# Performance work log

Measured on AMD Instinct MI355X. Metric: run time of the kernel, lower is better.

## Reference

```python
import jax, jax.numpy as jnp
import numpy as np

B, T, C = 8, 2048, 1024
HEAD = 64


def setup_inputs() -> dict:
    key = jax.random.key(0)
    kx, kk, kq, kv = jax.random.split(key, 4)
    scale = 1.0 / np.sqrt(C)
    x = jax.random.normal(kx, (B, T, C), dtype=jnp.float32)
    # nn.Linear(n_embd, head_size, bias=False) weight shape: (head_size, n_embd)
    Wk = jax.random.normal(kk, (HEAD, C), dtype=jnp.float32) * scale
    Wq = jax.random.normal(kq, (HEAD, C), dtype=jnp.float32) * scale
    Wv = jax.random.normal(kv, (HEAD, C), dtype=jnp.float32) * scale
    return {"x": x, "Wk": Wk, "Wq": Wq, "Wv": Wv}


def reference(x, Wk, Wq, Wv):
    Bb, Tt, Cc = x.shape
    k = jnp.einsum('btc,hc->bth', x, Wk)  # (B,T,head)
    q = jnp.einsum('btc,hc->bth', x, Wq)
    v = jnp.einsum('btc,hc->bth', x, Wv)
    scaling = Cc ** (-0.5)  # NOTE: scales by full embed dim C, per source
    wei = jnp.einsum('bth,bsh->bts', q, k) * scaling  # (B,T,T)
    causal = jnp.tril(jnp.ones((Tt, Tt), dtype=bool))
    wei = jnp.where(causal, wei, -jnp.inf)
    wei = jax.nn.softmax(wei, axis=-1)  # stable max-subtract softmax (= _safe_softmax)
    out = jnp.einsum('bts,bsh->bth', wei, v)  # (B,T,head)
    return out
```

## Files before the change

### kernel.cpp

```cpp
#include <hip/hip_runtime.h>
#include <math.h>

#define B_ 8
#define T_ 2048
#define C_ 1024
#define H_ 64
#define M_ (B_ * T_)

typedef short bf8 __attribute__((ext_vector_type(8)));
typedef float f32x4 __attribute__((ext_vector_type(4)));

__device__ __forceinline__ unsigned short f2b(float f) {
    unsigned u = __float_as_uint(f);
    u += 0x7fffu + ((u >> 16) & 1u);
    return (unsigned short)(u >> 16);
}
__device__ __forceinline__ float b2f(unsigned short u) {
    return __uint_as_float(((unsigned)u) << 16);
}
__device__ __forceinline__ unsigned pack2(float lo, float hi) {
    unsigned a = __float_as_uint(lo) + 0x8000u;
    unsigned b = __float_as_uint(hi) + 0x8000u;
    return __builtin_amdgcn_perm(b, a, 0x07060302u);
}

__global__ __launch_bounds__(256) void wconv_kernel(
    const float* __restrict__ Wk, const float* __restrict__ Wq,
    const float* __restrict__ Wv, unsigned short* __restrict__ wP)
{
    int gid = blockIdx.x * 256 + threadIdx.x;
    int l   = gid & 63;
    int kk  = (gid >> 6) & 31;
    int jg  = gid >> 11;
    int m15 = l & 15, q4 = l >> 4;
    int n   = 16 * jg + m15;
    int c0  = 32 * kk + 8 * q4;
    const float* src;
    float scl;
    if (n < 64)       { src = Wq + (size_t)n * C_ + c0;        scl = 0.03125f; }
    else if (n < 128) { src = Wk + (size_t)(n - 64) * C_ + c0; scl = 1.0f; }
    else              { src = Wv + (size_t)(n - 128) * C_ + c0; scl = 1.0f; }
    float4 a = *(const float4*)src;
    float4 b = *(const float4*)(src + 4);
    ushort4 o0 = make_ushort4(f2b(a.x * scl), f2b(a.y * scl), f2b(a.z * scl), f2b(a.w * scl));
    ushort4 o1 = make_ushort4(f2b(b.x * scl), f2b(b.y * scl), f2b(b.z * scl), f2b(b.w * scl));
    *(ushort4*)(wP + (size_t)gid * 8)     = o0;
    *(ushort4*)(wP + (size_t)gid * 8 + 4) = o1;
}

__global__ __launch_bounds__(256) void qkv_kernel(
    const float* __restrict__ x, const unsigned short* __restrict__ wP,
    unsigned short* __restrict__ qo, unsigned short* __restrict__ kP,
    unsigned short* __restrict__ vP)
{
    __shared__ unsigned short As[2][32 * 64];

    const int tid  = threadIdx.x;
    const int lane = tid & 63;
    const int w    = tid >> 6;
    const int m15  = lane & 15;
    const int q4   = lane >> 4;
    const int r0   = blockIdx.x * 32;

    const int arow = tid >> 3;
    const int aoct = tid & 7;
    const float* xp = x + (size_t)(r0 + arow) * C_ + aoct * 8;
    const int awo = arow * 64 + ((aoct ^ (arow & 7)) * 8);

    const unsigned short* wbase = wP + ((size_t)(3 * w) * 2048 + lane) * 8;

    f32x4 acc[2][3];
#pragma unroll
    for (int i = 0; i < 2; ++i)
#pragma unroll
        for (int j = 0; j < 3; ++j) acc[i][j] = f32x4{0.f, 0.f, 0.f, 0.f};

    float4 xa0 = *(const float4*)xp;
    float4 xa1 = *(const float4*)(xp + 4);
    bf8 wreg[3][2];
#pragma unroll
    for (int j = 0; j < 3; ++j)
#pragma unroll
        for (int kc = 0; kc < 2; ++kc)
            wreg[j][kc] = *(const bf8*)(wbase + ((size_t)j * 2048 + kc * 64) * 8);

    {
        uint4 u = {pack2(xa0.x, xa0.y), pack2(xa0.z, xa0.w),
                   pack2(xa1.x, xa1.y), pack2(xa1.z, xa1.w)};
        *(uint4*)&As[0][awo] = u;
    }

    const int swz = m15 & 7;
    for (int ck = 0; ck < 16; ++ck) {
        const int nxt = ck + 1;
        float4 xb0, xb1;
        bf8 wn[3][2];
        if (nxt < 16) {
            xb0 = *(const float4*)(xp + nxt * 64);
            xb1 = *(const float4*)(xp + nxt * 64 + 4);
#pragma unroll
            for (int j = 0; j < 3; ++j)
#pragma unroll
                for (int kc = 0; kc < 2; ++kc)
                    wn[j][kc] = *(const bf8*)(wbase + ((size_t)j * 2048 + (2 * nxt + kc) * 64) * 8);
        }
        __syncthreads();
        const int buf = ck & 1;
#pragma unroll
        for (int kc = 0; kc < 2; ++kc) {
            bf8 af[2];
#pragma unroll
            for (int i = 0; i < 2; ++i)
                af[i] = *(const bf8*)&As[buf][(16 * i + m15) * 64 + (((4 * kc + q4) ^ swz) * 8)];
#pragma unroll
            for (int i = 0; i < 2; ++i)
#pragma unroll
                for (int j = 0; j < 3; ++j)
                    acc[i][j] = __builtin_amdgcn_mfma_f32_16x16x32_bf16(
                        af[i], wreg[j][kc], acc[i][j], 0, 0, 0);
        }
        if (nxt < 16) {
            uint4 u = {pack2(xb0.x, xb0.y), pack2(xb0.z, xb0.w),
                       pack2(xb1.x, xb1.y), pack2(xb1.z, xb1.w)};
            *(uint4*)&As[nxt & 1][awo] = u;
#pragma unroll
            for (int j = 0; j < 3; ++j)
#pragma unroll
                for (int kc = 0; kc < 2; ++kc) wreg[j][kc] = wn[j][kc];
        }
    }

#pragma unroll
    for (int i = 0; i < 2; ++i) {
#pragma unroll
        for (int j = 0; j < 3; ++j) {
            const int base = 48 * w + 16 * j;
            if (base < 64) {
#pragma unroll
                for (int r = 0; r < 4; ++r) {
                    int t = r0 + 16 * i + 4 * q4 + r;
                    qo[(size_t)t * H_ + base + m15] = f2b(acc[i][j][r]);
                }
            } else if (base < 128) {
                const int D0 = base - 64;
                const int f  = D0 >> 5;
                const int c1 = (D0 >> 3) & 3;
                const int l2 = (c1 + (m15 >> 3)) * 16;
#pragma unroll
                for (int r = 0; r < 4; ++r) {
                    int t  = r0 + 16 * i + 4 * q4 + r;
                    int bb = t >> 11, tt = t & 2047;
                    kP[(size_t)bb * 131072 +
                       (size_t)((((tt >> 4) * 2 + f) * 64 + l2 + (tt & 15)) * 8 + (m15 & 7))]
                        = f2b(acc[i][j][r]);
                }
            } else {
                const int cg = (base - 128) >> 4;
#pragma unroll
                for (int r = 0; r < 4; ++r) {
                    int t  = r0 + 16 * i + 4 * q4 + r;
                    int bb = t >> 11, tt = t & 2047;
                    int lv = ((tt & 31) >> 3) * 16 + m15;
                    vP[(size_t)bb * 131072 +
                       (size_t)((((tt >> 5) * 4 + cg) * 64 + lv) * 8 + (tt & 7))]
                        = f2b(acc[i][j][r]);
                }
            }
        }
    }
}

__global__ __launch_bounds__(512) void attn_kernel(
    const unsigned short* __restrict__ qo, const unsigned short* __restrict__ kP,
    const unsigned short* __restrict__ vP, float* __restrict__ outp)
{
    __shared__ unsigned short Pl[8][2][16 * 64];
    __shared__ float Ml[2][4][2][16];
    __shared__ unsigned short Ob[2][3][2][16 * 64];

    const int tid  = threadIdx.x;
    const int lane = tid & 63;
    const int w    = tid >> 6;
    const int m15  = lane & 15;
    const int q4   = lane >> 4;
    const int b    = blockIdx.x;
    const int y    = blockIdx.y;
    const int gsel = w >> 2;
    const int s    = w & 3;
    const int g    = gsel ? (63 - y) : y;
    const int trow = 32 * g;
    const int last = g >> 1;

    const unsigned short* qb = qo + (size_t)b * T_ * H_;
    const unsigned short* kb = kP + (size_t)b * 131072;
    const unsigned short* vb = vP + (size_t)b * 131072;

    bf8 qf[2][2];
#pragma unroll
    for (int gq = 0; gq < 2; ++gq)
#pragma unroll
        for (int f = 0; f < 2; ++f)
            qf[gq][f] = *(const bf8*)(qb + (size_t)(trow + 16 * gq + m15) * H_ + 32 * f + 8 * q4);

    f32x4 o[2][4];
#pragma unroll
    for (int gq = 0; gq < 2; ++gq)
#pragma unroll
        for (int cg = 0; cg < 4; ++cg) o[gq][cg] = f32x4{0.f, 0.f, 0.f, 0.f};
    float lr[2] = {0.f, 0.f};

    bf8 kf[4][2];
    if (s <= last) {
#pragma unroll
        for (int t2 = 0; t2 < 4; ++t2)
#pragma unroll
            for (int f = 0; f < 2; ++f)
                kf[t2][f] = *(const bf8*)(kb + (size_t)(((4 * s + t2) * 2 + f) * 64 + lane) * 8);
    }

    const int swz = m15 & 7;
    for (int kt = s; kt <= last; kt += 4) {
        const bool more = (kt + 4 <= last);
        bf8 kn[4][2];
        if (more) {
#pragma unroll
            for (int t2 = 0; t2 < 4; ++t2)
#pragma unroll
                for (int f = 0; f < 2; ++f)
                    kn[t2][f] = *(const bf8*)(kb + (size_t)(((4 * (kt + 4) + t2) * 2 + f) * 64 + lane) * 8);
        }
        bf8 vf[2][4];
#pragma unroll
        for (int kc = 0; kc < 2; ++kc)
#pragma unroll
            for (int cg = 0; cg < 4; ++cg)
                vf[kc][cg] = *(const bf8*)(vb + (size_t)(((2 * kt + kc) * 4 + cg) * 64 + lane) * 8);

#pragma unroll
        for (int gq = 0; gq < 2; ++gq) {
            f32x4 sa[4];
#pragma unroll
            for (int t2 = 0; t2 < 4; ++t2) sa[t2] = f32x4{0.f, 0.f, 0.f, 0.f};
#pragma unroll
            for (int t2 = 0; t2 < 4; ++t2)
#pragma unroll
                for (int f = 0; f < 2; ++f)
                    sa[t2] = __builtin_amdgcn_mfma_f32_16x16x32_bf16(
                        kf[t2][f], qf[gq][f], sa[t2], 0, 0, 0);

            if (kt == last) {
#pragma unroll
                for (int t2 = 0; t2 < 4; ++t2)
#pragma unroll
                    for (int r = 0; r < 4; ++r)
                        if (64 * kt + 16 * t2 + 4 * q4 + r > trow + 16 * gq + m15)
                            sa[t2][r] = -INFINITY;
            }

            float p[4][4];
            float sum = 0.f;
#pragma unroll
            for (int t2 = 0; t2 < 4; ++t2)
#pragma unroll
                for (int r = 0; r < 4; ++r) {
                    p[t2][r] = __expf(sa[t2][r]);
                    sum += p[t2][r];
                }
            lr[gq] += sum;

#pragma unroll
            for (int t2 = 0; t2 < 4; ++t2) {
                uint2 pk = {pack2(p[t2][0], p[t2][1]), pack2(p[t2][2], p[t2][3])};
                int c = 2 * t2 + (q4 >> 1);
                *(uint2*)&Pl[w][gq][m15 * 64 + ((c ^ swz) * 8) + (q4 & 1) * 4] = pk;
            }
            bf8 pf[2];
#pragma unroll
            for (int kc = 0; kc < 2; ++kc)
                pf[kc] = *(const bf8*)&Pl[w][gq][m15 * 64 + (((4 * kc + q4) ^ swz) * 8)];

#pragma unroll
            for (int cg = 0; cg < 4; ++cg) {
                o[gq][cg] = __builtin_amdgcn_mfma_f32_16x16x32_bf16(
                    pf[0], vf[0][cg], o[gq][cg], 0, 0, 0);
                o[gq][cg] = __builtin_amdgcn_mfma_f32_16x16x32_bf16(
                    pf[1], vf[1][cg], o[gq][cg], 0, 0, 0);
            }
        }

        if (more) {
#pragma unroll
            for (int t2 = 0; t2 < 4; ++t2)
#pragma unroll
                for (int f = 0; f < 2; ++f) kf[t2][f] = kn[t2][f];
        }
    }

#pragma unroll
    for (int gq = 0; gq < 2; ++gq) {
        lr[gq] += __shfl_xor(lr[gq], 16);
        lr[gq] += __shfl_xor(lr[gq], 32);
    }
    if (q4 == 0) {
#pragma unroll
        for (int gq = 0; gq < 2; ++gq) Ml[gsel][s][gq][m15] = lr[gq];
    }
    if (s >= 1) {
#pragma unroll
        for (int gq = 0; gq < 2; ++gq)
#pragma unroll
            for (int cg = 0; cg < 4; ++cg)
#pragma unroll
                for (int r = 0; r < 4; ++r)
                    Ob[gsel][s - 1][gq][(4 * q4 + r) * 64 + 16 * cg + m15] = f2b(o[gq][cg][r]);
    }
    __syncthreads();
    if (s == 0) {
        float* op = outp + (size_t)(b * T_ + trow) * H_;
#pragma unroll
        for (int gq = 0; gq < 2; ++gq) {
#pragma unroll
            for (int r = 0; r < 4; ++r) {
                const int qq = 4 * q4 + r;
                float L = Ml[gsel][0][gq][qq] + Ml[gsel][1][gq][qq]
                        + Ml[gsel][2][gq][qq] + Ml[gsel][3][gq][qq];
                float inv = 1.0f / L;
#pragma unroll
                for (int cg = 0; cg < 4; ++cg) {
                    float a = o[gq][cg][r];
#pragma unroll
                    for (int i = 1; i < 4; ++i)
                        a += b2f(Ob[gsel][i - 1][gq][qq * 64 + 16 * cg + m15]);
                    op[(size_t)(16 * gq + qq) * H_ + 16 * cg + m15] = a * inv;
                }
            }
        }
    }
}

extern "C" void kernel_launch(void* const* d_in, const int* in_sizes, int n_in,
                              void* d_out, int out_size, void* d_ws, size_t ws_size,
                              hipStream_t stream) {
    const float* x  = (const float*)d_in[0];
    const float* Wk = (const float*)d_in[1];
    const float* Wq = (const float*)d_in[2];
    const float* Wv = (const float*)d_in[3];
    char* ws = (char*)d_ws;
    unsigned short* wP = (unsigned short*)ws;
    unsigned short* qo = (unsigned short*)(ws + 0x080000);
    unsigned short* kP = (unsigned short*)(ws + 0x280000);
    unsigned short* vP = (unsigned short*)(ws + 0x480000);

    wconv_kernel<<<96, 256, 0, stream>>>(Wk, Wq, Wv, wP);
    qkv_kernel<<<M_ / 32, 256, 0, stream>>>(x, wP, qo, kP, vP);
    attn_kernel<<<dim3(8, 32), 512, 0, stream>>>(qo, kP, vP, (float*)d_out);
}
```

Measured before the change: 125.0 us.

## Fuse weight conversion, QKV projection and attention into one cooperative kernel

Merges the three kernels into a single cooperative kernel of 256 blocks with 512 threads, separated by grid-wide syncs, to remove two kernel launch gaps. The QKV stage is retiled so each block covers 64 rows with 8 waves instead of 32 rows with 4 waves, which adds an extra __syncthreads per k-step. Grid.sync costs and the reduced QKV parallelism (256 blocks instead of 512) may offset the launch savings.

```diff
diff --git a/kernel.cpp b/kernel.cpp
--- a/kernel.cpp
+++ b/kernel.cpp
@@ -1,5 +1,8 @@
 #include <hip/hip_runtime.h>
+#include <hip/hip_cooperative_groups.h>
 #include <math.h>
+
+namespace cg = cooperative_groups;
 
 #define B_ 8
 #define T_ 2048
@@ -24,314 +27,312 @@
     return __builtin_amdgcn_perm(b, a, 0x07060302u);
 }
 
-__global__ __launch_bounds__(256) void wconv_kernel(
-    const float* __restrict__ Wk, const float* __restrict__ Wq,
-    const float* __restrict__ Wv, unsigned short* __restrict__ wP)
+__global__ __launch_bounds__(512) void fused_kernel(
+    const float* __restrict__ x, const float* __restrict__ Wk,
+    const float* __restrict__ Wq, const float* __restrict__ Wv,
+    unsigned short* __restrict__ wP, unsigned short* __restrict__ qo,
+    unsigned short* __restrict__ kP, unsigned short* __restrict__ vP,
+    float* __restrict__ outp)
 {
-    int gid = blockIdx.x * 256 + threadIdx.x;
-    int l   = gid & 63;
-    int kk  = (gid >> 6) & 31;
-    int jg  = gid >> 11;
-    int m15 = l & 15, q4 = l >> 4;
-    int n   = 16 * jg + m15;
-    int c0  = 32 * kk + 8 * q4;
-    const float* src;
-    float scl;
-    if (n < 64)       { src = Wq + (size_t)n * C_ + c0;        scl = 0.03125f; }
-    else if (n < 128) { src = Wk + (size_t)(n - 64) * C_ + c0; scl = 1.0f; }
-    else              { src = Wv + (size_t)(n - 128) * C_ + c0; scl = 1.0f; }
-    float4 a = *(const float4*)src;
-    float4 b = *(const float4*)(src + 4);
-    ushort4 o0 = make_ushort4(f2b(a.x * scl), f2b(a.y * scl), f2b(a.z * scl), f2b(a.w * scl));
-    ushort4 o1 = make_ushort4(f2b(b.x * scl), f2b(b.y * scl), f2b(b.z * scl), f2b(b.w * scl));
-    *(ushort4*)(wP + (size_t)gid * 8)     = o0;
-    *(ushort4*)(wP + (size_t)gid * 8 + 4) = o1;
-}
-
-__global__ __launch_bounds__(256) void qkv_kernel(
-    const float* __restrict__ x, const unsigned short* __restrict__ wP,
-    unsigned short* __restrict__ qo, unsigned short* __restrict__ kP,
-    unsigned short* __restrict__ vP)
-{
-    __shared__ unsigned short As[2][32 * 64];
-
+    __shared__ unsigned short As[2][64 * 64];
+    __shared__ unsigned short Pl[8][2][16 * 64];
+    __shared__ float Ml[2][4][2][16];
+    __shared__ unsigned short Ob[2][3][2][16 * 64];
+
+    cg::grid_group grid = cg::this_grid();
+    const int bid  = blockIdx.x;
     const int tid  = threadIdx.x;
     const int lane = tid & 63;
     const int w    = tid >> 6;
     const int m15  = lane & 15;
     const int q4   = lane >> 4;
-    const int r0   = blockIdx.x * 32;
-
-    const int arow = tid >> 3;
-    const int aoct = tid & 7;
-    const float* xp = x + (size_t)(r0 + arow) * C_ + aoct * 8;
-    const int awo = arow * 64 + ((aoct ^ (arow & 7)) * 8);
-
-    const unsigned short* wbase = wP + ((size_t)(3 * w) * 2048 + lane) * 8;
-
-    f32x4 acc[2][3];
-#pragma unroll
-    for (int i = 0; i < 2; ++i)
-#pragma unroll
-        for (int j = 0; j < 3; ++j) acc[i][j] = f32x4{0.f, 0.f, 0.f, 0.f};
-
-    float4 xa0 = *(const float4*)xp;
-    float4 xa1 = *(const float4*)(xp + 4);
-    bf8 wreg[3][2];
-#pragma unroll
-    for (int j = 0; j < 3; ++j)
-#pragma unroll
-        for (int kc = 0; kc < 2; ++kc)
-            wreg[j][kc] = *(const bf8*)(wbase + ((size_t)j * 2048 + kc * 64) * 8);
 
     {
-        uint4 u = {pack2(xa0.x, xa0.y), pack2(xa0.z, xa0.w),
-                   pack2(xa1.x, xa1.y), pack2(xa1.z, xa1.w)};
-        *(uint4*)&As[0][awo] = u;
+        int gid = bid * 512 + tid;
+        if (gid < 24576) {
+            int l   = gid & 63;
+            int kk  = (gid >> 6) & 31;
+            int jg  = gid >> 11;
+            int n   = 16 * jg + (l & 15);
+            int c0  = 32 * kk + 8 * (l >> 4);
+            const float* src;
+            float scl;
+            if (n < 64)       { src = Wq + (size_t)n * C_ + c0;         scl = 0.03125f; }
+            else if (n < 128) { src = Wk + (size_t)(n - 64) * C_ + c0;  scl = 1.0f; }
+            else              { src = Wv + (size_t)(n - 128) * C_ + c0; scl = 1.0f; }
+            float4 a = *(const float4*)src;
+            float4 b = *(const float4*)(src + 4);
+            *(ushort4*)(wP + (size_t)gid * 8) =
+                make_ushort4(f2b(a.x * scl), f2b(a.y * scl), f2b(a.z * scl), f2b(a.w * scl));
+            *(ushort4*)(wP + (size_t)gid * 8 + 4) =
+                make_ushort4(f2b(b.x * scl), f2b(b.y * scl), f2b(b.z * scl), f2b(b.w * scl));
+        }
     }
-
-    const int swz = m15 & 7;
-    for (int ck = 0; ck < 16; ++ck) {
-        const int nxt = ck + 1;
-        float4 xb0, xb1;
-        bf8 wn[3][2];
-        if (nxt < 16) {
-            xb0 = *(const float4*)(xp + nxt * 64);
-            xb1 = *(const float4*)(xp + nxt * 64 + 4);
-#pragma unroll
-            for (int j = 0; j < 3; ++j)
+    grid.sync();
+
+    {
+        const int wr = w >> 2;
+        const int wc = w & 3;
+        const int r0 = bid * 64;
+
+        const int arow = tid >> 3;
+        const int aoct = tid & 7;
+        const float* xp = x + (size_t)(r0 + arow) * C_ + aoct * 8;
+        const int awo = arow * 64 + ((aoct ^ (arow & 7)) * 8);
+
+        const unsigned short* wbase = wP + ((size_t)(3 * wc) * 2048 + lane) * 8;
+
+        f32x4 acc[2][3];
+#pragma unroll
+        for (int i = 0; i < 2; ++i)
+#pragma unroll
+            for (int j = 0; j < 3; ++j) acc[i][j] = f32x4{0.f, 0.f, 0.f, 0.f};
+
+        float4 xa0 = *(const float4*)xp;
+        float4 xa1 = *(const float4*)(xp + 4);
+        bf8 wreg[3][2];
+#pragma unroll
+        for (int j = 0; j < 3; ++j)
+#pragma unroll
+            for (int kc = 0; kc < 2; ++kc)
+                wreg[j][kc] = *(const bf8*)(wbase + ((size_t)j * 2048 + kc * 64) * 8);
+
+        *(uint4*)&As[0][awo] = uint4{pack2(xa0.x, xa0.y), pack2(xa0.z, xa0.w),
+                                     pack2(xa1.x, xa1.y), pack2(xa1.z, xa1.w)};
+
+        const int swz = m15 & 7;
+        for (int ck = 0; ck < 16; ++ck) {
+            const int nxt = ck + 1;
+            float4 xb0, xb1;
+            bf8 wn[3][2];
+            if (nxt < 16) {
+                xb0 = *(const float4*)(xp + nxt * 64);
+                xb1 = *(const float4*)(xp + nxt * 64 + 4);
+#pragma unroll
+                for (int j = 0; j < 3; ++j)
+#pragma unroll
+                    for (int kc = 0; kc < 2; ++kc)
+                        wn[j][kc] = *(const bf8*)(wbase + ((size_t)j * 2048 + (2 * nxt + kc) * 64) * 8);
+            }
+            __syncthreads();
+            const int buf = ck & 1;
+#pragma unroll
+            for (int kc = 0; kc < 2; ++kc) {
+                bf8 af[2];
+#pragma unroll
+                for (int i = 0; i < 2; ++i)
+                    af[i] = *(const bf8*)&As[buf][(32 * wr + 16 * i + m15) * 64 +
+                                                  (((4 * kc + q4) ^ swz) * 8)];
+#pragma unroll
+                for (int i = 0; i < 2; ++i)
+#pragma unroll
+                    for (int j = 0; j < 3; ++j)
+                        acc[i][j] = __builtin_amdgcn_mfma_f32_16x16x32_bf16(
+                            af[i], wreg[j][kc], acc[i][j], 0, 0, 0);
+            }
+            if (nxt < 16) {
+                __syncthreads();
+                *(uint4*)&As[nxt & 1][awo] = uint4{pack2(xb0.x, xb0.y), pack2(xb0.z, xb0.w),
+                                                   pack2(xb1.x, xb1.y), pack2(xb1.z, xb1.w)};
+#pragma unroll
+                for (int j = 0; j < 3; ++j)
+#pragma unroll
+                    for (int kc = 0; kc < 2; ++kc) wreg[j][kc] = wn[j][kc];
+            }
+        }
+
+#pragma unroll
+        for (int i = 0; i < 2; ++i) {
+#pragma unroll
+            for (int j = 0; j < 3; ++j) {
+                const int base = 48 * wc + 16 * j;
+                if (base < 64) {
+#pragma unroll
+                    for (int r = 0; r < 4; ++r) {
+                        int t = r0 + 32 * wr + 16 * i + 4 * q4 + r;
+                        qo[(size_t)t * H_ + base + m15] = f2b(acc[i][j][r]);
+                    }
+                } else if (base < 128) {
+                    const int D0 = base - 64;
+                    const int f  = D0 >> 5;
+                    const int c1 = (D0 >> 3) & 3;
+                    const int l2 = (c1 + (m15 >> 3)) * 16;
+#pragma unroll
+                    for (int r = 0; r < 4; ++r) {
+                        int t  = r0 + 32 * wr + 16 * i + 4 * q4 + r;
+                        int bb = t >> 11, tt = t & 2047;
+                        kP[(size_t)bb * 131072 +
+                           (size_t)((((tt >> 4) * 2 + f) * 64 + l2 + (tt & 15)) * 8 + (m15 & 7))]
+                            = f2b(acc[i][j][r]);
+                    }
+                } else {
+                    const int cg2 = (base - 128) >> 4;
+#pragma unroll
+                    for (int r = 0; r < 4; ++r) {
+                        int t  = r0 + 32 * wr + 16 * i + 4 * q4 + r;
+                        int bb = t >> 11, tt = t & 2047;
+                        int lv = ((tt & 31) >> 3) * 16 + m15;
+                        vP[(size_t)bb * 131072 +
+                           (size_t)((((tt >> 5) * 4 + cg2) * 64 + lv) * 8 + (tt & 7))]
+                            = f2b(acc[i][j][r]);
+                    }
+                }
+            }
+        }
+    }
+    grid.sync();
+
+    {
+        const int b    = bid & 7;
+        const int y    = bid >> 3;
+        const int gsel = w >> 2;
+        const int s    = w & 3;
+        const int g    = gsel ? (63 - y) : y;
+        const int trow = 32 * g;
+        const int last = g >> 1;
+
+        const unsigned short* qb = qo + (size_t)b * T_ * H_;
+        const unsigned short* kb = kP + (size_t)b * 131072;
+        const unsigned short* vb = vP + (size_t)b * 131072;
+
+        bf8 qf[2][2];
+#pragma unroll
+        for (int gq = 0; gq < 2; ++gq)
+#pragma unroll
+            for (int f = 0; f < 2; ++f)
+                qf[gq][f] = *(const bf8*)(qb + (size_t)(trow + 16 * gq + m15) * H_ + 32 * f + 8 * q4);
+
+        f32x4 o[2][4];
+#pragma unroll
+        for (int gq = 0; gq < 2; ++gq)
+#pragma unroll
+            for (int cg2 = 0; cg2 < 4; ++cg2) o[gq][cg2] = f32x4{0.f, 0.f, 0.f, 0.f};
+        float lr[2] = {0.f, 0.f};
+
+        bf8 kf[4][2];
+        if (s <= last) {
+#pragma unroll
+            for (int t2 = 0; t2 < 4; ++t2)
+#pragma unroll
+                for (int f = 0; f < 2; ++f)
+                    kf[t2][f] = *(const bf8*)(kb + (size_t)(((4 * s + t2) * 2 + f) * 64 + lane) * 8);
+        }
+
+        const int swz = m15 & 7;
+        for (int kt = s; kt <= last; kt += 4) {
+            const bool more = (kt + 4 <= last);
+            bf8 kn[4][2];
+            if (more) {
+#pragma unroll
+                for (int t2 = 0; t2 < 4; ++t2)
+#pragma unroll
+                    for (int f = 0; f < 2; ++f)
+                        kn[t2][f] = *(const bf8*)(kb + (size_t)(((4 * (kt + 4) + t2) * 2 + f) * 64 + lane) * 8);
+            }
+            bf8 vf[2][4];
+#pragma unroll
+            for (int kc = 0; kc < 2; ++kc)
+#pragma unroll
+                for (int cg2 = 0; cg2 < 4; ++cg2)
+                    vf[kc][cg2] = *(const bf8*)(vb + (size_t)(((2 * kt + kc) * 4 + cg2) * 64 + lane) * 8);
+
+#pragma unroll
+            for (int gq = 0; gq < 2; ++gq) {
+                f32x4 sa[4];
+#pragma unroll
+                for (int t2 = 0; t2 < 4; ++t2) sa[t2] = f32x4{0.f, 0.f, 0.f, 0.f};
+#pragma unroll
+                for (int t2 = 0; t2 < 4; ++t2)
+#pragma unroll
+                    for (int f = 0; f < 2; ++f)
+                        sa[t2] = __builtin_amdgcn_mfma_f32_16x16x32_bf16(
+                            kf[t2][f], qf[gq][f], sa[t2], 0, 0, 0);
+
+                if (kt == last) {
+#pragma unroll
+                    for (int t2 = 0; t2 < 4; ++t2)
+#pragma unroll
+                        for (int r = 0; r < 4; ++r)
+                            if (64 * kt + 16 * t2 + 4 * q4 + r > trow + 16 * gq + m15)
+                                sa[t2][r] = -INFINITY;
+                }
+
+                float p[4][4];
+                float sum = 0.f;
+#pragma unroll
+                for (int t2 = 0; t2 < 4; ++t2)
+#pragma unroll
+                    for (int r = 0; r < 4; ++r) {
+                        p[t2][r] = __expf(sa[t2][r]);
+                        sum += p[t2][r];
+                    }
+                lr[gq] += sum;
+
+#pragma unroll
+                for (int t2 = 0; t2 < 4; ++t2) {
+                    uint2 pk = {pack2(p[t2][0], p[t2][1]), pack2(p[t2][2], p[t2][3])};
+                    int c = 2 * t2 + (q4 >> 1);
+                    *(uint2*)&Pl[w][gq][m15 * 64 + ((c ^ swz) * 8) + (q4 & 1) * 4] = pk;
+                }
+                bf8 pf[2];
 #pragma unroll
                 for (int kc = 0; kc < 2; ++kc)
-                    wn[j][kc] = *(const bf8*)(wbase + ((size_t)j * 2048 + (2 * nxt + kc) * 64) * 8);
+                    pf[kc] = *(const bf8*)&Pl[w][gq][m15 * 64 + (((4 * kc + q4) ^ swz) * 8)];
+
+#pragma unroll
+                for (int cg2 = 0; cg2 < 4; ++cg2) {
+                    o[gq][cg2] = __builtin_amdgcn_mfma_f32_16x16x32_bf16(
+                        pf[0], vf[0][cg2], o[gq][cg2], 0, 0, 0);
+                    o[gq][cg2] = __builtin_amdgcn_mfma_f32_16x16x32_bf16(
+                        pf[1], vf[1][cg2], o[gq][cg2], 0, 0, 0);
+                }
+            }
+
+            if (more) {
+#pragma unroll
+                for (int t2 = 0; t2 < 4; ++t2)
+#pragma unroll
+                    for (int f = 0; f < 2; ++f) kf[t2][f] = kn[t2][f];
+            }
+        }
+
+#pragma unroll
+        for (int gq = 0; gq < 2; ++gq) {
+            lr[gq] += __shfl_xor(lr[gq], 16);
+            lr[gq] += __shfl_xor(lr[gq], 32);
+        }
+        if (q4 == 0) {
+#pragma unroll
+            for (int gq = 0; gq < 2; ++gq) Ml[gsel][s][gq][m15] = lr[gq];
+        }
+        if (s >= 1) {
+#pragma unroll
+            for (int gq = 0; gq < 2; ++gq)
+#pragma unroll
+                for (int cg2 = 0; cg2 < 4; ++cg2)
+#pragma unroll
+                    for (int r = 0; r < 4; ++r)
+                        Ob[gsel][s - 1][gq][(4 * q4 + r) * 64 + 16 * cg2 + m15] = f2b(o[gq][cg2][r]);
         }
         __syncthreads();
-        const int buf = ck & 1;
-#pragma unroll
-        for (int kc = 0; kc < 2; ++kc) {
-            bf8 af[2];
-#pragma unroll
-            for (int i = 0; i < 2; ++i)
-                af[i] = *(const bf8*)&As[buf][(16 * i + m15) * 64 + (((4 * kc + q4) ^ swz) * 8)];
-#pragma unroll
-            for (int i = 0; i < 2; ++i)
-#pragma unroll
-                for (int j = 0; j < 3; ++j)
-                    acc[i][j] = __builtin_amdgcn_mfma_f32_16x16x32_bf16(
-                        af[i], wreg[j][kc], acc[i][j], 0, 0, 0);
-        }
-        if (nxt < 16) {
-            uint4 u = {pack2(xb0.x, xb0.y), pack2(xb0.z, xb0.w),
-                       pack2(xb1.x, xb1.y), pack2(xb1.z, xb1.w)};
-            *(uint4*)&As[nxt & 1][awo] = u;
-#pragma unroll
-            for (int j = 0; j < 3; ++j)
-#pragma unroll
-                for (int kc = 0; kc < 2; ++kc) wreg[j][kc] = wn[j][kc];
-        }
-    }
-
-#pragma unroll
-    for (int i = 0; i < 2; ++i) {
-#pragma unroll
-        for (int j = 0; j < 3; ++j) {
-            const int base = 48 * w + 16 * j;
-            if (base < 64) {
+        if (s == 0) {
+            float* op = outp + (size_t)(b * T_ + trow) * H_;
+#pragma unroll
+            for (int gq = 0; gq < 2; ++gq) {
 #pragma unroll
                 for (int r = 0; r < 4; ++r) {
-                    int t = r0 + 16 * i + 4 * q4 + r;
-                    qo[(size_t)t * H_ + base + m15] = f2b(acc[i][j][r]);
-                }
-            } else if (base < 128) {
-                const int D0 = base - 64;
-                const int f  = D0 >> 5;
-                const int c1 = (D0 >> 3) & 3;
-                const int l2 = (c1 + (m15 >> 3)) * 16;
-#pragma unroll
-                for (int r = 0; r < 4; ++r) {
-                    int t  = r0 + 16 * i + 4 * q4 + r;
-                    int bb = t >> 11, tt = t & 2047;
-                    kP[(size_t)bb * 131072 +
-                       (size_t)((((tt >> 4) * 2 + f) * 64 + l2 + (tt & 15)) * 8 + (m15 & 7))]
-                        = f2b(acc[i][j][r]);
-                }
-            } else {
-                const int cg = (base - 128) >> 4;
-#pragma unroll
-                for (int r = 0; r < 4; ++r) {
-                    int t  = r0 + 16 * i + 4 * q4 + r;
-                    int bb = t >> 11, tt = t & 2047;
-                    int lv = ((tt & 31) >> 3) * 16 + m15;
-                    vP[(size_t)bb * 131072 +
-                       (size_t)((((tt >> 5) * 4 + cg) * 64 + lv) * 8 + (tt & 7))]
-                        = f2b(acc[i][j][r]);
-                }
-            }
-        }
-    }
-}
-
-__global__ __launch_bounds__(512) void attn_kernel(
-    const unsigned short* __restrict__ qo, const unsigned short* __restrict__ kP,
-    const unsigned short* __restrict__ vP, float* __restrict__ outp)
-{
-    __shared__ unsigned short Pl[8][2][16 * 64];
-    __shared__ float Ml[2][4][2][16];
-    __shared__ unsigned short Ob[2][3][2][16 * 64];
-
-    const int tid  = threadIdx.x;
-    const int lane = tid & 63;
-    const int w    = tid >> 6;
-    const int m15  = lane & 15;
-    const int q4   = lane >> 4;
-    const int b    = blockIdx.x;
-    const int y    = blockIdx.y;
-    const int gsel = w >> 2;
-    const int s    = w & 3;
-    const int g    = gsel ? (63 - y) : y;
-    const int trow = 32 * g;
-    const int last = g >> 1;
-
-    const unsigned short* qb = qo + (size_t)b * T_ * H_;
-    const unsigned short* kb = kP + (size_t)b * 131072;
-    const unsigned short* vb = vP + (size_t)b * 131072;
-
-    bf8 qf[2][2];
-#pragma unroll
-    for (int gq = 0; gq < 2; ++gq)
-#pragma unroll
-        for (int f = 0; f < 2; ++f)
-            qf[gq][f] = *(const bf8*)(qb + (size_t)(trow + 16 * gq + m15) * H_ + 32 * f + 8 * q4);
-
-    f32x4 o[2][4];
-#pragma unroll
-    for (int gq = 0; gq < 2; ++gq)
-#pragma unroll
-        for (int cg = 0; cg < 4; ++cg) o[gq][cg] = f32x4{0.f, 0.f, 0.f, 0.f};
-    float lr[2] = {0.f, 0.f};
-
-    bf8 kf[4][2];
-    if (s <= last) {
-#pragma unroll
-        for (int t2 = 0; t2 < 4; ++t2)
-#pragma unroll
-            for (int f = 0; f < 2; ++f)
-                kf[t2][f] = *(const bf8*)(kb + (size_t)(((4 * s + t2) * 2 + f) * 64 + lane) * 8);
-    }
-
-    const int swz = m15 & 7;
-    for (int kt = s; kt <= last; kt += 4) {
-        const bool more = (kt + 4 <= last);
-        bf8 kn[4][2];
-        if (more) {
-#pragma unroll
-            for (int t2 = 0; t2 < 4; ++t2)
-#pragma unroll
-                for (int f = 0; f < 2; ++f)
-                    kn[t2][f] = *(const bf8*)(kb + (size_t)(((4 * (kt + 4) + t2) * 2 + f) * 64 + lane) * 8);
-        }
-        bf8 vf[2][4];
-#pragma unroll
-        for (int kc = 0; kc < 2; ++kc)
-#pragma unroll
-            for (int cg = 0; cg < 4; ++cg)
-                vf[kc][cg] = *(const bf8*)(vb + (size_t)(((2 * kt + kc) * 4 + cg) * 64 + lane) * 8);
-
-#pragma unroll
-        for (int gq = 0; gq < 2; ++gq) {
-            f32x4 sa[4];
-#pragma unroll
-            for (int t2 = 0; t2 < 4; ++t2) sa[t2] = f32x4{0.f, 0.f, 0.f, 0.f};
-#pragma unroll
-            for (int t2 = 0; t2 < 4; ++t2)
-#pragma unroll
-                for (int f = 0; f < 2; ++f)
-                    sa[t2] = __builtin_amdgcn_mfma_f32_16x16x32_bf16(
-                        kf[t2][f], qf[gq][f], sa[t2], 0, 0, 0);
-
-            if (kt == last) {
-#pragma unroll
-                for (int t2 = 0; t2 < 4; ++t2)
-#pragma unroll
-                    for (int r = 0; r < 4; ++r)
-                        if (64 * kt + 16 * t2 + 4 * q4 + r > trow + 16 * gq + m15)
-                            sa[t2][r] = -INFINITY;
-            }
-
-            float p[4][4];
-            float sum = 0.f;
-#pragma unroll
-            for (int t2 = 0; t2 < 4; ++t2)
-#pragma unroll
-                for (int r = 0; r < 4; ++r) {
-                    p[t2][r] = __expf(sa[t2][r]);
-                    sum += p[t2][r];
-                }
-            lr[gq] += sum;
-
-#pragma unroll
-            for (int t2 = 0; t2 < 4; ++t2) {
-                uint2 pk = {pack2(p[t2][0], p[t2][1]), pack2(p[t2][2], p[t2][3])};
-                int c = 2 * t2 + (q4 >> 1);
-                *(uint2*)&Pl[w][gq][m15 * 64 + ((c ^ swz) * 8) + (q4 & 1) * 4] = pk;
-            }
-            bf8 pf[2];
-#pragma unroll
-            for (int kc = 0; kc < 2; ++kc)
-                pf[kc] = *(const bf8*)&Pl[w][gq][m15 * 64 + (((4 * kc + q4) ^ swz) * 8)];
-
-#pragma unroll
-            for (int cg = 0; cg < 4; ++cg) {
-                o[gq][cg] = __builtin_amdgcn_mfma_f32_16x16x32_bf16(
-                    pf[0], vf[0][cg], o[gq][cg], 0, 0, 0);
-                o[gq][cg] = __builtin_amdgcn_mfma_f32_16x16x32_bf16(
-                    pf[1], vf[1][cg], o[gq][cg], 0, 0, 0);
-            }
-        }
-
-        if (more) {
-#pragma unroll
-            for (int t2 = 0; t2 < 4; ++t2)
-#pragma unroll
-                for (int f = 0; f < 2; ++f) kf[t2][f] = kn[t2][f];
-        }
-    }
-
-#pragma unroll
-    for (int gq = 0; gq < 2; ++gq) {
-        lr[gq] += __shfl_xor(lr[gq], 16);
-        lr[gq] += __shfl_xor(lr[gq], 32);
-    }
-    if (q4 == 0) {
-#pragma unroll
-        for (int gq = 0; gq < 2; ++gq) Ml[gsel][s][gq][m15] = lr[gq];
-    }
-    if (s >= 1) {
-#pragma unroll
-        for (int gq = 0; gq < 2; ++gq)
-#pragma unroll
-            for (int cg = 0; cg < 4; ++cg)
-#pragma unroll
-                for (int r = 0; r < 4; ++r)
-                    Ob[gsel][s - 1][gq][(4 * q4 + r) * 64 + 16 * cg + m15] = f2b(o[gq][cg][r]);
-    }
-    __syncthreads();
-    if (s == 0) {
-        float* op = outp + (size_t)(b * T_ + trow) * H_;
-#pragma unroll
-        for (int gq = 0; gq < 2; ++gq) {
-#pragma unroll
-            for (int r = 0; r < 4; ++r) {
-                const int qq = 4 * q4 + r;
-                float L = Ml[gsel][0][gq][qq] + Ml[gsel][1][gq][qq]
-                        + Ml[gsel][2][gq][qq] + Ml[gsel][3][gq][qq];
-                float inv = 1.0f / L;
-#pragma unroll
-                for (int cg = 0; cg < 4; ++cg) {
-                    float a = o[gq][cg][r];
-#pragma unroll
-                    for (int i = 1; i < 4; ++i)
-                        a += b2f(Ob[gsel][i - 1][gq][qq * 64 + 16 * cg + m15]);
-                    op[(size_t)(16 * gq + qq) * H_ + 16 * cg + m15] = a * inv;
+                    const int qq = 4 * q4 + r;
+                    float L = Ml[gsel][0][gq][qq] + Ml[gsel][1][gq][qq]
+                            + Ml[gsel][2][gq][qq] + Ml[gsel][3][gq][qq];
+                    float inv = 1.0f / L;
+#pragma unroll
+                    for (int cg2 = 0; cg2 < 4; ++cg2) {
+                        float a = o[gq][cg2][r];
+#pragma unroll
+                        for (int i = 1; i < 4; ++i)
+                            a += b2f(Ob[gsel][i - 1][gq][qq * 64 + 16 * cg2 + m15]);
+                        op[(size_t)(16 * gq + qq) * H_ + 16 * cg2 + m15] = a * inv;
+                    }
                 }
             }
         }
@@ -345,13 +346,14 @@
     const float* Wk = (const float*)d_in[1];
     const float* Wq = (const float*)d_in[2];
     const float* Wv = (const float*)d_in[3];
+    float* out = (float*)d_out;
     char* ws = (char*)d_ws;
     unsigned short* wP = (unsigned short*)ws;
     unsigned short* qo = (unsigned short*)(ws + 0x080000);
     unsigned short* kP = (unsigned short*)(ws + 0x280000);
     unsigned short* vP = (unsigned short*)(ws + 0x480000);
 
-    wconv_kernel<<<96, 256, 0, stream>>>(Wk, Wq, Wv, wP);
-    qkv_kernel<<<M_ / 32, 256, 0, stream>>>(x, wP, qo, kP, vP);
-    attn_kernel<<<dim3(8, 32), 512, 0, stream>>>(qo, kP, vP, (float*)d_out);
-}
+    void* args[] = {&x, &Wk, &Wq, &Wv, &wP, &qo, &kP, &vP, &out};
+    hipLaunchCooperativeKernel((const void*)fused_kernel, dim3(256), dim3(512),
+                               args, 0, stream);
+}
```

After: 191.5 us. +53.3%, slower.
